# Performance work log

Measured on AMD Instinct MI355X. Metric: run time of the kernel, lower is better.

Reference implementation:

```python
import jax, jax.numpy as jnp
import numpy as np

B, S, N = 16, 512, 321          # batch, input length, n_variates (dec_in)
D, DF, LAYERS = 512, 2048, 2    # d_model, d_ff, e_layers
M, K, P = 3, 3, 96              # wavelet levels, kernel_size, pred_len
ALPHA = 0.3


def _dwconv(x, h, dilation):
    # x: [B, C, L], h: [C, K] depthwise dilated conv (cross-correlation, like torch)
    return jax.lax.conv_general_dilated(
        x, h[:, None, :], window_strides=(1,), padding='VALID',
        rhs_dilation=(dilation,), dimension_numbers=('NCH', 'OIH', 'NCH'),
        feature_group_count=x.shape[1])


def _swt_dec(x, h0, h1):
    # stationary wavelet decomposition; x: [B, N, D] -> [B, N, M+1, D]
    approx, coeffs, dil = x, [], 1
    for _ in range(M):
        pad_total = dil * (K - 1)
        pad_r = (K * dil) // 2
        xp = jnp.pad(approx, ((0, 0), (0, 0), (pad_total - pad_r, pad_r)), mode='wrap')
        coeffs.append(_dwconv(xp, h1, dil))
        approx = _dwconv(xp, h0, dil)
        dil *= 2
    coeffs.append(approx)
    return jnp.stack(coeffs[::-1], axis=-2)


def _swt_rec(c, g0, g1):
    # inverse SWT; c: [B, N, M+1, D] -> [B, N, D]
    approx = c[:, :, 0, :]
    dil = 2 ** (M - 1)
    for i in range(M):
        det = c[:, :, 1 + i, :]
        pad_total = dil * (K - 1)
        pad_l = (dil * K) // 2
        pads = ((0, 0), (0, 0), (pad_l, pad_total - pad_l))
        approx = (_dwconv(jnp.pad(approx, pads, mode='wrap'), g0, dil)
                  + _dwconv(jnp.pad(det, pads, mode='wrap'), g1, dil)) / 2
        dil //= 2
    return approx


def _geom_attention(q, k, v):
    # q,k,v: [B, L=D, H=M+1, E=N]
    scale = 1.0 / jnp.sqrt(jnp.float32(q.shape[-1]))
    dot = jnp.einsum('blhe,bshe->bhls', q, k)
    qn2 = jnp.sum(q * q, -1).transpose(0, 2, 1)  # [B,H,L]
    kn2 = jnp.sum(k * k, -1).transpose(0, 2, 1)  # [B,H,S]
    wedge = jnp.sqrt(jax.nn.relu(qn2[:, :, :, None] * kn2[:, :, None, :] - dot * dot) + 1e-8)
    scores = ((1.0 - ALPHA) * dot + ALPHA * wedge) * scale
    A = jax.nn.softmax(scores, axis=-1)
    return jnp.einsum('bhls,bshd->blhd', A, v)


def _layernorm(x, g, b, eps=1e-5):
    mu = x.mean(-1, keepdims=True)
    var = jnp.mean((x - mu) ** 2, -1, keepdims=True)
    return (x - mu) / jnp.sqrt(var + eps) * g + b


def _forward(x_enc, emb_W, emb_b, h0, h1, g0, g1, Wq, bq, Wk, bk, Wv, bv, Wo, bo,
             W1, b1, W2, b2, ln1_g, ln1_b, ln2_g, ln2_b, lnf_g, lnf_b, proj_W, proj_b):
    # RevIN-style normalize (means detached as in torch code)
    means = jax.lax.stop_gradient(x_enc.mean(1, keepdims=True))
    stdev = jnp.sqrt(x_enc.var(1, keepdims=True) + 1e-5)
    x = (x_enc - means) / stdev
    # inverted embedding: each variate's full series -> d_model token
    h = jnp.einsum('bsn,ds->bnd', x, emb_W) + emb_b  # [B,N,D]
    for l in range(LAYERS):
        coeffs = _swt_dec(h, h0[l], h1[l])  # [B,N,M+1,D]
        q = (jnp.einsum('bnmd,ed->bnme', coeffs, Wq[l]) + bq[l]).transpose(0, 3, 2, 1)
        kk = (jnp.einsum('bnmd,ed->bnme', coeffs, Wk[l]) + bk[l]).transpose(0, 3, 2, 1)
        vv = (jnp.einsum('bnmd,ed->bnme', coeffs, Wv[l]) + bv[l]).transpose(0, 3, 2, 1)
        out = _geom_attention(q, kk, vv).transpose(0, 3, 2, 1)  # [B,N,M+1,D]
        out = _swt_rec(out, g0[l], g1[l])                        # [B,N,D]
        out = jnp.einsum('bnd,ed->bne', out, Wo[l]) + bo[l]
        x1 = _layernorm(h + out, ln1_g[l], ln1_b[l])
        y = jax.nn.gelu(jnp.einsum('bnd,fd->bnf', x1, W1[l]) + b1[l], approximate=False)
        y = jnp.einsum('bnf,df->bnd', y, W2[l]) + b2[l]
        h = _layernorm(x1 + y, ln2_g[l], ln2_b[l])
    h = _layernorm(h, lnf_g, lnf_b)
    dec = (jnp.einsum('bnd,pd->bnp', h, proj_W) + proj_b).transpose(0, 2, 1)  # [B,P,N]
    dec = dec * stdev[:, 0, :][:, None, :] + means[:, 0, :][:, None, :]
    return dec, means, stdev


def setup_inputs():
    key = jax.random.key(0)
    ks = jax.random.split(key, 24)
    def filt(k):
        f = jax.random.normal(k, (LAYERS, N, K), jnp.float32)
        return f / jnp.linalg.norm(f, axis=-1, keepdims=True)
    w = lambda k, shape: jax.random.normal(k, shape, jnp.float32) * 0.02
    z = lambda shape: jnp.zeros(shape, jnp.float32)
    o = lambda shape: jnp.ones(shape, jnp.float32)
    return {
        'x_enc': jax.random.normal(ks[0], (B, S, N), jnp.float32),
        'emb_W': w(ks[1], (D, S)), 'emb_b': z((D,)),
        'h0': filt(ks[2]), 'h1': filt(ks[3]), 'g0': filt(ks[4]), 'g1': filt(ks[5]),
        'Wq': w(ks[6], (LAYERS, D, D)), 'bq': z((LAYERS, D)),
        'Wk': w(ks[7], (LAYERS, D, D)), 'bk': z((LAYERS, D)),
        'Wv': w(ks[8], (LAYERS, D, D)), 'bv': z((LAYERS, D)),
        'Wo': w(ks[9], (LAYERS, D, D)), 'bo': z((LAYERS, D)),
        'W1': w(ks[10], (LAYERS, DF, D)), 'b1': z((LAYERS, DF)),
        'W2': w(ks[11], (LAYERS, D, DF)), 'b2': z((LAYERS, D)),
        'ln1_g': o((LAYERS, D)), 'ln1_b': z((LAYERS, D)),
        'ln2_g': o((LAYERS, D)), 'ln2_b': z((LAYERS, D)),
        'lnf_g': o((D,)), 'lnf_b': z((D,)),
        'proj_W': w(ks[12], (P, D)), 'proj_b': z((P,)),
    }


def reference(x_enc, emb_W, emb_b, h0, h1, g0, g1, Wq, bq, Wk, bk, Wv, bv, Wo, bo,
              W1, b1, W2, b2, ln1_g, ln1_b, ln2_g, ln2_b, lnf_g, lnf_b, proj_W, proj_b):
    return _forward(x_enc, emb_W, emb_b, h0, h1, g0, g1, Wq, bq, Wk, bk, Wv, bv, Wo, bo,
                    W1, b1, W2, b2, ln1_g, ln1_b, ln2_g, ln2_b, lnf_g, lnf_b, proj_W, proj_b)
```

## Files before the change

kernel.cpp:

```cpp
#include <hip/hip_runtime.h>
#include <hip/hip_bf16.h>
#include <math.h>
#include <stdint.h>

#define Bn 16
#define Sn 512
#define Nn 321
#define Dn 512
#define DFn 2048
#define Pn 96
#define KP 352

typedef __bf16 bf16x8 __attribute__((ext_vector_type(8)));
typedef float f32x4 __attribute__((ext_vector_type(4)));
typedef __hip_bfloat16 bf16;

static __device__ __forceinline__ float gelu_exact(float x) {
    return 0.5f * x * (1.0f + erff(x * 0.7071067811865476f));
}

static __device__ __forceinline__ void gld16(const void* g, void* l) {
    __builtin_amdgcn_global_load_lds(
        (const __attribute__((address_space(1))) void*)(uintptr_t)g,
        (__attribute__((address_space(3))) void*)(uintptr_t)l, 16, 0, 0);
}

struct CvtPack {
    const float* src[14];
    bf16* dst[14];
    int cnt[14];
};
__global__ void cvt_all_kernel(CvtPack p) {
    int seg = blockIdx.y;
    int n = p.cnt[seg];
    const float* s = p.src[seg];
    bf16* d = p.dst[seg];
    int i = (blockIdx.x * 256 + threadIdx.x) * 4;
    if (i + 3 < n) {
        float4 v = *reinterpret_cast<const float4*>(s + i);
        d[i] = __float2bfloat16(v.x);
        d[i + 1] = __float2bfloat16(v.y);
        d[i + 2] = __float2bfloat16(v.z);
        d[i + 3] = __float2bfloat16(v.w);
    }
}

__global__ void stats_kernel(const float* __restrict__ x, float* __restrict__ means,
                             float* __restrict__ stdev) {
    int b = blockIdx.y;
    int n = blockIdx.x * 256 + threadIdx.x;
    if (n >= Nn) return;
    const float* p = x + (size_t)b * Sn * Nn + n;
    float s = 0.f, s2 = 0.f;
    for (int ss = 0; ss < Sn; ++ss) { float v = p[(size_t)ss * Nn]; s += v; s2 += v * v; }
    float mu = s * (1.0f / Sn);
    float var = s2 * (1.0f / Sn) - mu * mu;
    means[b * Nn + n] = mu;
    stdev[b * Nn + n] = sqrtf(var + 1e-5f);
}

__global__ void transpose_norm_kernel(const float* __restrict__ x,
                                      const float* __restrict__ means,
                                      const float* __restrict__ stdev,
                                      bf16* __restrict__ xT) {
    __shared__ float tile[32][33];
    int b = blockIdx.z;
    int s0 = blockIdx.x * 32, n0 = blockIdx.y * 32;
    int tx = threadIdx.x, ty = threadIdx.y;
#pragma unroll
    for (int u = 0; u < 4; ++u) {
        int srow = ty + u * 8;
        int n = n0 + tx;
        tile[srow][tx] = (n < Nn) ? x[((size_t)b * Sn + (s0 + srow)) * Nn + n] : 0.f;
    }
    __syncthreads();
#pragma unroll
    for (int u = 0; u < 4; ++u) {
        int n = n0 + ty + u * 8;
        int s = s0 + tx;
        if (n < Nn) {
            float mu = means[b * Nn + n], sd = stdev[b * Nn + n];
            xT[((size_t)b * Nn + n) * Sn + s] = __float2bfloat16((tile[tx][ty + u * 8] - mu) / sd);
        }
    }
}

template <int OUT, int EPI>
__global__ __launch_bounds__(256) void mm_kernel(
    const bf16* __restrict__ A, const bf16* __restrict__ Bm,
    const float* __restrict__ bias, void* __restrict__ C,
    int Mdim, int Ndim, int Kdim, int lda, int ldb, int ldc,
    long sAi, long sAo, long sBi, long sBo, long sCi, long sCo, int innerB) {
    int z = blockIdx.z;
    int zi = z % innerB, zo = z / innerB;
    const bf16* Ab = A + (size_t)zi * sAi + (size_t)zo * sAo;
    const bf16* Bb = Bm + (size_t)zi * sBi + (size_t)zo * sBo;
    __shared__ __align__(16) bf16 As[128 * 32];
    __shared__ __align__(16) bf16 Bs[128 * 32];
    int t = threadIdx.x;
    int wave = t >> 6, lane = t & 63;
    int wr = wave >> 1, wc = wave & 1;
    int q = lane >> 4, l16 = lane & 15;
    int i0 = blockIdx.y * 128, j0 = blockIdx.x * 128;

    int srow0 = t >> 2;
    int scol = (t & 3) * 8;
    f32x4 acc[4][4] = {};

    for (int k0 = 0; k0 < Kdim; k0 += 32) {
#pragma unroll
        for (int u = 0; u < 2; ++u) {
            int row = u * 64 + srow0;
            int gcol = scol ^ (((row >> 1) & 3) << 3);
            int gi = i0 + row; if (gi >= Mdim) gi = Mdim - 1;
            gld16(Ab + (size_t)gi * lda + k0 + gcol, &As[u * 2048 + wave * 512]);
            int gj = j0 + row; if (gj >= Ndim) gj = Ndim - 1;
            gld16(Bb + (size_t)gj * ldb + k0 + gcol, &Bs[u * 2048 + wave * 512]);
        }
        __syncthreads();
        bf16x8 af[4], bfr[4];
#pragma unroll
        for (int mi = 0; mi < 4; ++mi) {
            int r = wr * 64 + mi * 16 + l16;
            int cl = (q * 8) ^ (((r >> 1) & 3) << 3);
            af[mi] = *reinterpret_cast<const bf16x8*>(&As[r * 32 + cl]);
        }
#pragma unroll
        for (int ni = 0; ni < 4; ++ni) {
            int r = wc * 64 + ni * 16 + l16;
            int cl = (q * 8) ^ (((r >> 1) & 3) << 3);
            bfr[ni] = *reinterpret_cast<const bf16x8*>(&Bs[r * 32 + cl]);
        }
#pragma unroll
        for (int mi = 0; mi < 4; ++mi)
#pragma unroll
            for (int ni = 0; ni < 4; ++ni)
                acc[mi][ni] = __builtin_amdgcn_mfma_f32_16x16x32_bf16(af[mi], bfr[ni], acc[mi][ni], 0, 0, 0);
        __syncthreads();
    }
    size_t cbase = (size_t)zi * sCi + (size_t)zo * sCo;
#pragma unroll
    for (int mi = 0; mi < 4; ++mi) {
#pragma unroll
        for (int r = 0; r < 4; ++r) {
            int gi = i0 + wr * 64 + mi * 16 + q * 4 + r;
            if (gi >= Mdim) continue;
#pragma unroll
            for (int ni = 0; ni < 4; ++ni) {
                int gj = j0 + wc * 64 + ni * 16 + l16;
                if (gj >= Ndim) continue;
                float v = acc[mi][ni][r];
                if (bias) v += bias[gj];
                if (EPI == 1) v = gelu_exact(v);
                size_t cidx = cbase + (size_t)gi * ldc + gj;
                if (OUT == 0) ((float*)C)[cidx] = v;
                else ((bf16*)C)[cidx] = __float2bfloat16(v);
            }
        }
    }
}

__global__ __launch_bounds__(128) void swt_dec_kernel(
    const float* __restrict__ h, const float* __restrict__ h0f,
    const float* __restrict__ h1f, bf16* __restrict__ coeffs) {
    __shared__ float a[2][512];
    int b = blockIdx.y, n = blockIdx.x, t = threadIdx.x;
    const float* hrow = h + ((size_t)b * Nn + n) * Dn;
#pragma unroll
    for (int u = 0; u < 4; ++u) a[0][t + u * 128] = hrow[t + u * 128];
    float f0[3], f1[3];
#pragma unroll
    for (int k = 0; k < 3; ++k) { f0[k] = h0f[n * 3 + k]; f1[k] = h1f[n * 3 + k]; }
    __syncthreads();
    bf16* cb = coeffs + ((size_t)b * Nn + n) * 4 * Dn;
    int cur = 0;
    for (int lev = 0; lev < 3; ++lev) {
        int dil = 1 << lev;
        int pl = 2 * dil - (3 * dil) / 2;
#pragma unroll
        for (int u = 0; u < 4; ++u) {
            int d = t + u * 128;
            float dv = 0.f, av = 0.f;
#pragma unroll
            for (int k = 0; k < 3; ++k) {
                int idx = (d + k * dil - pl) & 511;
                float xv = a[cur][idx];
                dv += f1[k] * xv;
                av += f0[k] * xv;
            }
            cb[(size_t)(3 - lev) * Dn + d] = __float2bfloat16(dv);
            a[cur ^ 1][d] = av;
        }
        __syncthreads();
        cur ^= 1;
    }
#pragma unroll
    for (int u = 0; u < 4; ++u) cb[t + u * 128] = __float2bfloat16(a[cur][t + u * 128]);
}

__global__ __launch_bounds__(128) void swt_rec_kernel(
    const bf16* __restrict__ attn, const float* __restrict__ g0f,
    const float* __restrict__ g1f, bf16* __restrict__ rec) {
    __shared__ float a[2][512];
    __shared__ float det[512];
    int b = blockIdx.y, n = blockIdx.x, t = threadIdx.x;
    const bf16* base = attn + ((size_t)(b * 4) * Nn + n) * Dn;
#pragma unroll
    for (int u = 0; u < 4; ++u) a[0][t + u * 128] = __bfloat162float(base[t + u * 128]);
    float w0[3], w1[3];
#pragma unroll
    for (int k = 0; k < 3; ++k) { w0[k] = g0f[n * 3 + k]; w1[k] = g1f[n * 3 + k]; }
    int cur = 0;
    for (int i = 0; i < 3; ++i) {
        int dil = 4 >> i;
        int pl = (3 * dil) / 2;
        const bf16* drow = base + (size_t)(1 + i) * Nn * Dn;
#pragma unroll
        for (int u = 0; u < 4; ++u) det[t + u * 128] = __bfloat162float(drow[t + u * 128]);
        __syncthreads();
#pragma unroll
        for (int u = 0; u < 4; ++u) {
            int d = t + u * 128;
            float s = 0.f;
#pragma unroll
            for (int k = 0; k < 3; ++k) {
                int idx = (d + k * dil - pl) & 511;
                s += w0[k] * a[cur][idx] + w1[k] * det[idx];
            }
            a[cur ^ 1][d] = s * 0.5f;
        }
        __syncthreads();
        cur ^= 1;
    }
    bf16* out = rec + ((size_t)b * Nn + n) * Dn;
#pragma unroll
    for (int u = 0; u < 4; ++u) out[t + u * 128] = __float2bfloat16(a[cur][t + u * 128]);
}

__global__ void tconv_kernel(const bf16* __restrict__ in, bf16* __restrict__ out) {
    __shared__ bf16 tile[32][33];
    int bm = blockIdx.z;
    int b = bm >> 2, m = bm & 3;
    int e0 = blockIdx.x * 32, n0 = blockIdx.y * 32;
    int tx = threadIdx.x, ty = threadIdx.y;
    const bf16* ib = in + (size_t)b * 4 * Nn * 512 + (size_t)m * 512;
    bf16* ob = out + (size_t)bm * 512 * KP;
#pragma unroll
    for (int u = 0; u < 4; ++u) {
        int n = n0 + ty + u * 8;
        bf16 v = __float2bfloat16(0.f);
        if (n < Nn) v = ib[(size_t)n * 2048 + e0 + tx];
        tile[ty + u * 8][tx] = v;
    }
    __syncthreads();
#pragma unroll
    for (int u = 0; u < 4; ++u) {
        int e = e0 + ty + u * 8;
        int n = n0 + tx;
        if (n < KP) ob[(size_t)e * KP + n] = tile[tx][ty + u * 8];
    }
}

__global__ __launch_bounds__(256) void colsq_kernel(const bf16* __restrict__ Q0,
                                                    float* __restrict__ outv) {
    int bm = blockIdx.y;
    int b = bm >> 2, m = bm & 3;
    int e0 = blockIdx.x * 64;
    int tx = threadIdx.x & 63, ty = threadIdx.x >> 6;
    const bf16* base = Q0 + ((size_t)b * Nn * 4 + m) * 512;
    float s = 0.f;
    for (int n = ty; n < Nn; n += 4) {
        float v = __bfloat162float(base[(size_t)n * 2048 + e0 + tx]);
        s += v * v;
    }
    __shared__ float red[4][64];
    red[ty][tx] = s;
    __syncthreads();
    if (ty == 0)
        outv[(size_t)bm * 512 + e0 + tx] = red[0][tx] + red[1][tx] + red[2][tx] + red[3][tx];
}

__global__ __launch_bounds__(256) void wedge_softmax_kernel(
    bf16* __restrict__ Smat, const float* __restrict__ qn2, const float* __restrict__ kn2) {
    int bm = blockIdx.y, l = blockIdx.x, t = threadIdx.x;
    bf16* row = Smat + ((size_t)bm * 512 + l) * 512;
    const float* kn = kn2 + (size_t)bm * 512;
    float q2 = qn2[(size_t)bm * 512 + l];
    const float scale = rsqrtf(321.0f);
    float v[2];
    float mx = -1e30f;
#pragma unroll
    for (int u = 0; u < 2; ++u) {
        int s = t + u * 256;
        float d = __bfloat162float(row[s]);
        float w = sqrtf(fmaxf(q2 * kn[s] - d * d, 0.f) + 1e-8f);
        float sc = (0.7f * d + 0.3f * w) * scale;
        v[u] = sc;
        mx = fmaxf(mx, sc);
    }
    __shared__ float red[256];
    red[t] = mx;
    __syncthreads();
    for (int o = 128; o > 0; o >>= 1) {
        if (t < o) red[t] = fmaxf(red[t], red[t + o]);
        __syncthreads();
    }
    mx = red[0];
    __syncthreads();
    float sum = 0.f;
#pragma unroll
    for (int u = 0; u < 2; ++u) {
        v[u] = expf(v[u] - mx);
        sum += v[u];
    }
    red[t] = sum;
    __syncthreads();
    for (int o = 128; o > 0; o >>= 1) {
        if (t < o) red[t] += red[t + o];
        __syncthreads();
    }
    float inv = 1.0f / red[0];
#pragma unroll
    for (int u = 0; u < 2; ++u) row[t + u * 256] = __float2bfloat16(v[u] * inv);
}

__global__ __launch_bounds__(128) void ln_kernel(
    const float* __restrict__ A, const float* __restrict__ R,
    const float* __restrict__ g, const float* __restrict__ bb,
    float* __restrict__ outf, bf16* __restrict__ outb) {
    size_t r = blockIdx.x;
    int t = threadIdx.x;
    const float* ra = A + r * Dn;
    float x[4];
    float s = 0.f, s2 = 0.f;
#pragma unroll
    for (int u = 0; u < 4; ++u) {
        int d = t + u * 128;
        float v = ra[d];
        if (R) v += R[r * Dn + d];
        x[u] = v;
        s += v;
        s2 += v * v;
    }
    __shared__ float rs[128], rs2[128];
    rs[t] = s;
    rs2[t] = s2;
    __syncthreads();
    for (int o = 64; o > 0; o >>= 1) {
        if (t < o) { rs[t] += rs[t + o]; rs2[t] += rs2[t + o]; }
        __syncthreads();
    }
    float mean = rs[0] * (1.0f / Dn);
    float var = rs2[0] * (1.0f / Dn) - mean * mean;
    float inv = rsqrtf(var + 1e-5f);
#pragma unroll
    for (int u = 0; u < 4; ++u) {
        int d = t + u * 128;
        float v = (x[u] - mean) * inv * g[d] + bb[d];
        if (outf) outf[r * Dn + d] = v;
        if (outb) outb[r * Dn + d] = __float2bfloat16(v);
    }
}

__global__ void out_scale_kernel(const float* __restrict__ ptmp,
                                 const float* __restrict__ means,
                                 const float* __restrict__ stdev, float* __restrict__ dec) {
    int idx = blockIdx.x * 256 + threadIdx.x;
    if (idx >= Bn * Pn * Nn) return;
    int n = idx % Nn;
    int bp = idx / Nn;
    int p = bp % Pn;
    int b = bp / Pn;
    float v = ptmp[((size_t)b * Nn + n) * Pn + p];
    dec[idx] = v * stdev[b * Nn + n] + means[b * Nn + n];
}

extern "C" void kernel_launch(void* const* d_in, const int* in_sizes, int n_in,
                              void* d_out, int out_size, void* d_ws, size_t ws_size,
                              hipStream_t stream) {
    const float* x_enc = (const float*)d_in[0];
    const float* emb_W = (const float*)d_in[1];
    const float* emb_b = (const float*)d_in[2];
    const float* h0 = (const float*)d_in[3];
    const float* h1 = (const float*)d_in[4];
    const float* g0 = (const float*)d_in[5];
    const float* g1 = (const float*)d_in[6];
    const float* Wq = (const float*)d_in[7];
    const float* bq = (const float*)d_in[8];
    const float* Wk = (const float*)d_in[9];
    const float* bk = (const float*)d_in[10];
    const float* Wv = (const float*)d_in[11];
    const float* bv = (const float*)d_in[12];
    const float* Wo = (const float*)d_in[13];
    const float* bo = (const float*)d_in[14];
    const float* W1 = (const float*)d_in[15];
    const float* b1 = (const float*)d_in[16];
    const float* W2 = (const float*)d_in[17];
    const float* b2 = (const float*)d_in[18];
    const float* ln1_g = (const float*)d_in[19];
    const float* ln1_b = (const float*)d_in[20];
    const float* ln2_g = (const float*)d_in[21];
    const float* ln2_b = (const float*)d_in[22];
    const float* lnf_g = (const float*)d_in[23];
    const float* lnf_b = (const float*)d_in[24];
    const float* proj_W = (const float*)d_in[25];
    const float* proj_b = (const float*)d_in[26];

    float* dec = (float*)d_out;
    float* means = dec + (size_t)Bn * Pn * Nn;
    float* stdev = means + (size_t)Bn * Nn;

    char* p = (char*)d_ws;
    auto alloc = [&](size_t bytes) { char* r = p; p += (bytes + 255) & ~(size_t)255; return r; };
    const size_t RD = (size_t)Bn * Nn * Dn;
    const size_t RQ4 = RD * 4;

    bf16* embWb = (bf16*)alloc(262144 * 2);
    bf16* Wqb = (bf16*)alloc(2 * 262144 * 2);
    bf16* Wkb = (bf16*)alloc(2 * 262144 * 2);
    bf16* Wvb = (bf16*)alloc(2 * 262144 * 2);
    bf16* Wob = (bf16*)alloc(2 * 262144 * 2);
    bf16* W1b = (bf16*)alloc(2 * 1048576 * 2);
    bf16* W2b = (bf16*)alloc(2 * 1048576 * 2);
    bf16* projWb = (bf16*)alloc(49152 * 2);

    float* hbuf = (float*)alloc(RD * 4);
    char* regC = alloc(RQ4 * 2);
    char* regQ = alloc(RQ4 * 2);
    char* regK = alloc(RQ4 * 2);
    char* regV = alloc(RQ4 * 2);
    char* regT = alloc((size_t)2 * 64 * 512 * KP * 2);
    float* qn2 = (float*)alloc(64 * 512 * 4);
    float* kn2 = (float*)alloc(64 * 512 * 4);

    bf16* coeffs_b = (bf16*)regC;
    bf16* attn_b = (bf16*)regC;
    bf16* Q0b = (bf16*)regQ;
    bf16* Smat = (bf16*)regQ;
    bf16* recb = (bf16*)regQ;
    bf16* x1b = (bf16*)(regQ + RD * 2);
    float* ptmp = (float*)regQ;
    bf16* K0b = (bf16*)regK;
    bf16* V0b = (bf16*)regV;
    bf16* yb = (bf16*)regV;
    bf16* Qt = (bf16*)regT;
    bf16* Kt = Qt + (size_t)64 * 512 * KP;
    bf16* xT_b = (bf16*)regT;
    float* x1 = (float*)regT;
    float* tmp = (float*)(regT + RD * 4);
    bf16* hfb = (bf16*)(regT + RD * 8);

    const int R = Bn * Nn;
    const int RQr = R * 4;
    const long sbm = (long)4 * Nn * 512;
    const long sS = (long)512 * 512;
    const long sTq = (long)512 * KP;
    const long sTb = 4 * sTq;

    CvtPack cp;
    int ci = 0;
    auto addcvt = [&](const float* s, bf16* d, int n) { cp.src[ci] = s; cp.dst[ci] = d; cp.cnt[ci] = n; ++ci; };
    addcvt(emb_W, embWb, 262144);
    for (int l = 0; l < 2; ++l) {
        addcvt(Wq + (size_t)l * 262144, Wqb + (size_t)l * 262144, 262144);
        addcvt(Wk + (size_t)l * 262144, Wkb + (size_t)l * 262144, 262144);
        addcvt(Wv + (size_t)l * 262144, Wvb + (size_t)l * 262144, 262144);
        addcvt(Wo + (size_t)l * 262144, Wob + (size_t)l * 262144, 262144);
        addcvt(W1 + (size_t)l * 1048576, W1b + (size_t)l * 1048576, 1048576);
        addcvt(W2 + (size_t)l * 1048576, W2b + (size_t)l * 1048576, 1048576);
    }
    addcvt(proj_W, projWb, 49152);
    cvt_all_kernel<<<dim3(1048576 / 4 / 256, 14), 256, 0, stream>>>(cp);

    stats_kernel<<<dim3((Nn + 255) / 256, Bn), 256, 0, stream>>>(x_enc, means, stdev);
    transpose_norm_kernel<<<dim3(Sn / 32, (Nn + 31) / 32, Bn), dim3(32, 8), 0, stream>>>(
        x_enc, means, stdev, xT_b);

    mm_kernel<0, 0><<<dim3(4, (R + 127) / 128, 1), 256, 0, stream>>>(
        xT_b, embWb, emb_b, hbuf, R, Dn, Sn, Sn, Sn, Dn, 0, 0, 0, 0, 0, 0, 1);

    for (int l = 0; l < 2; ++l) {
        const float* h0l = h0 + (size_t)l * Nn * 3;
        const float* h1l = h1 + (size_t)l * Nn * 3;
        const float* g0l = g0 + (size_t)l * Nn * 3;
        const float* g1l = g1 + (size_t)l * Nn * 3;

        swt_dec_kernel<<<dim3(Nn, Bn), 128, 0, stream>>>(hbuf, h0l, h1l, coeffs_b);

        mm_kernel<1, 0><<<dim3(4, (RQr + 127) / 128, 1), 256, 0, stream>>>(
            coeffs_b, Wqb + (size_t)l * 262144, bq + (size_t)l * Dn, Q0b,
            RQr, Dn, Dn, Dn, Dn, Dn, 0, 0, 0, 0, 0, 0, 1);
        mm_kernel<1, 0><<<dim3(4, (RQr + 127) / 128, 1), 256, 0, stream>>>(
            coeffs_b, Wkb + (size_t)l * 262144, bk + (size_t)l * Dn, K0b,
            RQr, Dn, Dn, Dn, Dn, Dn, 0, 0, 0, 0, 0, 0, 1);
        mm_kernel<1, 0><<<dim3(4, (RQr + 127) / 128, 1), 256, 0, stream>>>(
            coeffs_b, Wvb + (size_t)l * 262144, bv + (size_t)l * Dn, V0b,
            RQr, Dn, Dn, Dn, Dn, Dn, 0, 0, 0, 0, 0, 0, 1);

        colsq_kernel<<<dim3(8, 64), 256, 0, stream>>>(Q0b, qn2);
        colsq_kernel<<<dim3(8, 64), 256, 0, stream>>>(K0b, kn2);
        tconv_kernel<<<dim3(16, 11, 64), dim3(32, 8), 0, stream>>>(Q0b, Qt);
        tconv_kernel<<<dim3(16, 11, 64), dim3(32, 8), 0, stream>>>(K0b, Kt);

        mm_kernel<1, 0><<<dim3(4, 4, 64), 256, 0, stream>>>(
            Qt, Kt, nullptr, Smat, 512, 512, KP, KP, KP, 512,
            sTq, sTb, sTq, sTb, sS, 4 * sS, 4);

        wedge_softmax_kernel<<<dim3(512, 64), 256, 0, stream>>>(Smat, qn2, kn2);

        mm_kernel<1, 0><<<dim3(4, (Nn + 127) / 128, 64), 256, 0, stream>>>(
            V0b, Smat, nullptr, attn_b, Nn, 512, 512, 2048, 512, 512,
            512, sbm, sS, 4 * sS, (long)Nn * 512, (long)4 * Nn * 512, 4);

        swt_rec_kernel<<<dim3(Nn, Bn), 128, 0, stream>>>(attn_b, g0l, g1l, recb);

        mm_kernel<0, 0><<<dim3(4, (R + 127) / 128, 1), 256, 0, stream>>>(
            recb, Wob + (size_t)l * 262144, bo + (size_t)l * Dn, tmp,
            R, Dn, Dn, Dn, Dn, Dn, 0, 0, 0, 0, 0, 0, 1);
        ln_kernel<<<R, 128, 0, stream>>>(hbuf, tmp, ln1_g + (size_t)l * Dn,
                                         ln1_b + (size_t)l * Dn, x1, x1b);

        mm_kernel<1, 1><<<dim3(16, (R + 127) / 128, 1), 256, 0, stream>>>(
            x1b, W1b + (size_t)l * 1048576, b1 + (size_t)l * DFn, yb,
            R, DFn, Dn, Dn, Dn, DFn, 0, 0, 0, 0, 0, 0, 1);
        mm_kernel<0, 0><<<dim3(4, (R + 127) / 128, 1), 256, 0, stream>>>(
            yb, W2b + (size_t)l * 1048576, b2 + (size_t)l * Dn, tmp,
            R, Dn, DFn, DFn, DFn, Dn, 0, 0, 0, 0, 0, 0, 1);
        ln_kernel<<<R, 128, 0, stream>>>(x1, tmp, ln2_g + (size_t)l * Dn,
                                         ln2_b + (size_t)l * Dn, hbuf, nullptr);
    }

    ln_kernel<<<R, 128, 0, stream>>>(hbuf, nullptr, lnf_g, lnf_b, nullptr, hfb);
    mm_kernel<0, 0><<<dim3(1, (R + 127) / 128, 1), 256, 0, stream>>>(
        hfb, projWb, proj_b, ptmp, R, Pn, Dn, Dn, Dn, Pn, 0, 0, 0, 0, 0, 0, 1);
    out_scale_kernel<<<(Bn * Pn * Nn + 255) / 256, 256, 0, stream>>>(ptmp, means, stdev, dec);
}
```

Before: 1.092 ms.

## Fuse Q/K projections into one GEMM and split-K narrow GEMMs

Wq and Wk are packed into one weight, with a packed bias, so one N=1024 GEMM produces an interleaved QK buffer. The column-norm and transpose kernels are merged to handle Q and K in a single launch each. The Wo, W2 and final projection GEMMs are split along K (2, 2 and 4 ways) into separate partial buffers. LayerNorm and the output-scaling kernel sum those partials. This targets launch overhead and the low block count of the narrow GEMMs, at the cost of extra partial-sum traffic and workspace, and a risk of the bias being added once per split.

Measured after the change: 1.003 ms. 1.09x faster.

```diff
diff --git a/kernel.cpp b/kernel.cpp
--- a/kernel.cpp
+++ b/kernel.cpp
@@ -45,6 +45,14 @@
     }
 }
 
+__global__ void bias_pack_kernel(const float* __restrict__ bq, const float* __restrict__ bk,
+                                 float* __restrict__ bqk) {
+    int idx = blockIdx.x * 256 + threadIdx.x;
+    if (idx >= 2048) return;
+    int l = idx >> 10, j = idx & 1023;
+    bqk[idx] = (j < 512) ? bq[l * 512 + j] : bk[l * 512 + j - 512];
+}
+
 __global__ void stats_kernel(const float* __restrict__ x, float* __restrict__ means,
                              float* __restrict__ stdev) {
     int b = blockIdx.y;
@@ -237,19 +245,20 @@
     for (int u = 0; u < 4; ++u) out[t + u * 128] = __float2bfloat16(a[cur][t + u * 128]);
 }
 
-__global__ void tconv_kernel(const bf16* __restrict__ in, bf16* __restrict__ out) {
+__global__ void tconv2_kernel(const bf16* __restrict__ QK, bf16* __restrict__ QtKt) {
     __shared__ bf16 tile[32][33];
-    int bm = blockIdx.z;
+    int zz = blockIdx.z;
+    int qk = zz >> 6, bm = zz & 63;
     int b = bm >> 2, m = bm & 3;
     int e0 = blockIdx.x * 32, n0 = blockIdx.y * 32;
     int tx = threadIdx.x, ty = threadIdx.y;
-    const bf16* ib = in + (size_t)b * 4 * Nn * 512 + (size_t)m * 512;
-    bf16* ob = out + (size_t)bm * 512 * KP;
+    const bf16* ib = QK + (size_t)b * Nn * 4096 + (size_t)m * 1024 + (size_t)qk * 512;
+    bf16* ob = QtKt + (size_t)qk * 64 * 512 * KP + (size_t)bm * 512 * KP;
 #pragma unroll
     for (int u = 0; u < 4; ++u) {
         int n = n0 + ty + u * 8;
         bf16 v = __float2bfloat16(0.f);
-        if (n < Nn) v = ib[(size_t)n * 2048 + e0 + tx];
+        if (n < Nn) v = ib[(size_t)n * 4096 + e0 + tx];
         tile[ty + u * 8][tx] = v;
     }
     __syncthreads();
@@ -261,23 +270,25 @@
     }
 }
 
-__global__ __launch_bounds__(256) void colsq_kernel(const bf16* __restrict__ Q0,
-                                                    float* __restrict__ outv) {
-    int bm = blockIdx.y;
+__global__ __launch_bounds__(256) void colsq2_kernel(const bf16* __restrict__ QK,
+                                                     float* __restrict__ outv) {
+    int y = blockIdx.y;
+    int qk = y >> 6, bm = y & 63;
     int b = bm >> 2, m = bm & 3;
     int e0 = blockIdx.x * 64;
     int tx = threadIdx.x & 63, ty = threadIdx.x >> 6;
-    const bf16* base = Q0 + ((size_t)b * Nn * 4 + m) * 512;
+    const bf16* base = QK + ((size_t)b * Nn * 4 + m) * 1024 + (size_t)qk * 512;
     float s = 0.f;
     for (int n = ty; n < Nn; n += 4) {
-        float v = __bfloat162float(base[(size_t)n * 2048 + e0 + tx]);
+        float v = __bfloat162float(base[(size_t)n * 4096 + e0 + tx]);
         s += v * v;
     }
     __shared__ float red[4][64];
     red[ty][tx] = s;
     __syncthreads();
     if (ty == 0)
-        outv[(size_t)bm * 512 + e0 + tx] = red[0][tx] + red[1][tx] + red[2][tx] + red[3][tx];
+        outv[(size_t)qk * 32768 + (size_t)bm * 512 + e0 + tx] =
+            red[0][tx] + red[1][tx] + red[2][tx] + red[3][tx];
 }
 
 __global__ __launch_bounds__(256) void wedge_softmax_kernel(
@@ -325,7 +336,7 @@
 }
 
 __global__ __launch_bounds__(128) void ln_kernel(
-    const float* __restrict__ A, const float* __restrict__ R,
+    const float* __restrict__ A, const float* __restrict__ R, const float* __restrict__ R2,
     const float* __restrict__ g, const float* __restrict__ bb,
     float* __restrict__ outf, bf16* __restrict__ outb) {
     size_t r = blockIdx.x;
@@ -338,6 +349,7 @@
         int d = t + u * 128;
         float v = ra[d];
         if (R) v += R[r * Dn + d];
+        if (R2) v += R2[r * Dn + d];
         x[u] = v;
         s += v;
         s2 += v * v;
@@ -371,7 +383,9 @@
     int bp = idx / Nn;
     int p = bp % Pn;
     int b = bp / Pn;
-    float v = ptmp[((size_t)b * Nn + n) * Pn + p];
+    const size_t PS = (size_t)Bn * Nn * Pn;
+    size_t base = ((size_t)b * Nn + n) * Pn + p;
+    float v = ptmp[base] + ptmp[base + PS] + ptmp[base + 2 * PS] + ptmp[base + 3 * PS];
     dec[idx] = v * stdev[b * Nn + n] + means[b * Nn + n];
 }
 
@@ -416,13 +430,13 @@
     const size_t RQ4 = RD * 4;
 
     bf16* embWb = (bf16*)alloc(262144 * 2);
-    bf16* Wqb = (bf16*)alloc(2 * 262144 * 2);
-    bf16* Wkb = (bf16*)alloc(2 * 262144 * 2);
+    bf16* Wqkb = (bf16*)alloc(2 * 524288 * 2);
     bf16* Wvb = (bf16*)alloc(2 * 262144 * 2);
     bf16* Wob = (bf16*)alloc(2 * 262144 * 2);
     bf16* W1b = (bf16*)alloc(2 * 1048576 * 2);
     bf16* W2b = (bf16*)alloc(2 * 1048576 * 2);
     bf16* projWb = (bf16*)alloc(49152 * 2);
+    float* bqk = (float*)alloc(2048 * 4);
 
     float* hbuf = (float*)alloc(RD * 4);
     char* regC = alloc(RQ4 * 2);
@@ -430,25 +444,25 @@
     char* regK = alloc(RQ4 * 2);
     char* regV = alloc(RQ4 * 2);
     char* regT = alloc((size_t)2 * 64 * 512 * KP * 2);
-    float* qn2 = (float*)alloc(64 * 512 * 4);
-    float* kn2 = (float*)alloc(64 * 512 * 4);
+    float* qn2 = (float*)alloc((size_t)2 * 64 * 512 * 4);
+    float* kn2 = qn2 + 32768;
 
     bf16* coeffs_b = (bf16*)regC;
     bf16* attn_b = (bf16*)regC;
-    bf16* Q0b = (bf16*)regQ;
+    bf16* QK0b = (bf16*)regQ;
     bf16* Smat = (bf16*)regQ;
     bf16* recb = (bf16*)regQ;
     bf16* x1b = (bf16*)(regQ + RD * 2);
     float* ptmp = (float*)regQ;
-    bf16* K0b = (bf16*)regK;
     bf16* V0b = (bf16*)regV;
     bf16* yb = (bf16*)regV;
-    bf16* Qt = (bf16*)regT;
-    bf16* Kt = Qt + (size_t)64 * 512 * KP;
+    bf16* QtKt = (bf16*)regT;
+    bf16* Qt = QtKt;
+    bf16* Kt = QtKt + (size_t)64 * 512 * KP;
     bf16* xT_b = (bf16*)regT;
     float* x1 = (float*)regT;
     float* tmp = (float*)(regT + RD * 4);
-    bf16* hfb = (bf16*)(regT + RD * 8);
+    bf16* hfb = (bf16*)(regT + RD * 12);
 
     const int R = Bn * Nn;
     const int RQr = R * 4;
@@ -462,8 +476,8 @@
     auto addcvt = [&](const float* s, bf16* d, int n) { cp.src[ci] = s; cp.dst[ci] = d; cp.cnt[ci] = n; ++ci; };
     addcvt(emb_W, embWb, 262144);
     for (int l = 0; l < 2; ++l) {
-        addcvt(Wq + (size_t)l * 262144, Wqb + (size_t)l * 262144, 262144);
-        addcvt(Wk + (size_t)l * 262144, Wkb + (size_t)l * 262144, 262144);
+        addcvt(Wq + (size_t)l * 262144, Wqkb + (size_t)l * 524288, 262144);
+        addcvt(Wk + (size_t)l * 262144, Wqkb + (size_t)l * 524288 + 262144, 262144);
         addcvt(Wv + (size_t)l * 262144, Wvb + (size_t)l * 262144, 262144);
         addcvt(Wo + (size_t)l * 262144, Wob + (size_t)l * 262144, 262144);
         addcvt(W1 + (size_t)l * 1048576, W1b + (size_t)l * 1048576, 1048576);
@@ -471,6 +485,7 @@
     }
     addcvt(proj_W, projWb, 49152);
     cvt_all_kernel<<<dim3(1048576 / 4 / 256, 14), 256, 0, stream>>>(cp);
+    bias_pack_kernel<<<8, 256, 0, stream>>>(bq, bk, bqk);
 
     stats_kernel<<<dim3((Nn + 255) / 256, Bn), 256, 0, stream>>>(x_enc, means, stdev);
     transpose_norm_kernel<<<dim3(Sn / 32, (Nn + 31) / 32, Bn), dim3(32, 8), 0, stream>>>(
@@ -487,20 +502,15 @@
 
         swt_dec_kernel<<<dim3(Nn, Bn), 128, 0, stream>>>(hbuf, h0l, h1l, coeffs_b);
 
-        mm_kernel<1, 0><<<dim3(4, (RQr + 127) / 128, 1), 256, 0, stream>>>(
-            coeffs_b, Wqb + (size_t)l * 262144, bq + (size_t)l * Dn, Q0b,
-            RQr, Dn, Dn, Dn, Dn, Dn, 0, 0, 0, 0, 0, 0, 1);
-        mm_kernel<1, 0><<<dim3(4, (RQr + 127) / 128, 1), 256, 0, stream>>>(
-            coeffs_b, Wkb + (size_t)l * 262144, bk + (size_t)l * Dn, K0b,
-            RQr, Dn, Dn, Dn, Dn, Dn, 0, 0, 0, 0, 0, 0, 1);
+        mm_kernel<1, 0><<<dim3(8, (RQr + 127) / 128, 1), 256, 0, stream>>>(
+            coeffs_b, Wqkb + (size_t)l * 524288, bqk + (size_t)l * 1024, QK0b,
+            RQr, 1024, Dn, Dn, Dn, 1024, 0, 0, 0, 0, 0, 0, 1);
         mm_kernel<1, 0><<<dim3(4, (RQr + 127) / 128, 1), 256, 0, stream>>>(
             coeffs_b, Wvb + (size_t)l * 262144, bv + (size_t)l * Dn, V0b,
             RQr, Dn, Dn, Dn, Dn, Dn, 0, 0, 0, 0, 0, 0, 1);
 
-        colsq_kernel<<<dim3(8, 64), 256, 0, stream>>>(Q0b, qn2);
-        colsq_kernel<<<dim3(8, 64), 256, 0, stream>>>(K0b, kn2);
-        tconv_kernel<<<dim3(16, 11, 64), dim3(32, 8), 0, stream>>>(Q0b, Qt);
-        tconv_kernel<<<dim3(16, 11, 64), dim3(32, 8), 0, stream>>>(K0b, Kt);
+        colsq2_kernel<<<dim3(8, 128), 256, 0, stream>>>(QK0b, qn2);
+        tconv2_kernel<<<dim3(16, 11, 128), dim3(32, 8), 0, stream>>>(QK0b, QtKt);
 
         mm_kernel<1, 0><<<dim3(4, 4, 64), 256, 0, stream>>>(
             Qt, Kt, nullptr, Smat, 512, 512, KP, KP, KP, 512,
@@ -514,24 +524,25 @@
 
         swt_rec_kernel<<<dim3(Nn, Bn), 128, 0, stream>>>(attn_b, g0l, g1l, recb);
 
-        mm_kernel<0, 0><<<dim3(4, (R + 127) / 128, 1), 256, 0, stream>>>(
+        mm_kernel<0, 0><<<dim3(4, (R + 127) / 128, 2), 256, 0, stream>>>(
             recb, Wob + (size_t)l * 262144, bo + (size_t)l * Dn, tmp,
-            R, Dn, Dn, Dn, Dn, Dn, 0, 0, 0, 0, 0, 0, 1);
-        ln_kernel<<<R, 128, 0, stream>>>(hbuf, tmp, ln1_g + (size_t)l * Dn,
+            R, Dn, 256, Dn, Dn, Dn, 256, 0, 256, 0, (long)RD, 0, 2);
+        ln_kernel<<<R, 128, 0, stream>>>(hbuf, tmp, tmp + RD, ln1_g + (size_t)l * Dn,
                                          ln1_b + (size_t)l * Dn, x1, x1b);
 
         mm_kernel<1, 1><<<dim3(16, (R + 127) / 128, 1), 256, 0, stream>>>(
             x1b, W1b + (size_t)l * 1048576, b1 + (size_t)l * DFn, yb,
             R, DFn, Dn, Dn, Dn, DFn, 0, 0, 0, 0, 0, 0, 1);
-        mm_kernel<0, 0><<<dim3(4, (R + 127) / 128, 1), 256, 0, stream>>>(
+        mm_kernel<0, 0><<<dim3(4, (R + 127) / 128, 2), 256, 0, stream>>>(
             yb, W2b + (size_t)l * 1048576, b2 + (size_t)l * Dn, tmp,
-            R, Dn, DFn, DFn, DFn, Dn, 0, 0, 0, 0, 0, 0, 1);
-        ln_kernel<<<R, 128, 0, stream>>>(x1, tmp, ln2_g + (size_t)l * Dn,
+            R, Dn, 1024, DFn, DFn, Dn, 1024, 0, 1024, 0, (long)RD, 0, 2);
+        ln_kernel<<<R, 128, 0, stream>>>(x1, tmp, tmp + RD, ln2_g + (size_t)l * Dn,
                                          ln2_b + (size_t)l * Dn, hbuf, nullptr);
     }
 
-    ln_kernel<<<R, 128, 0, stream>>>(hbuf, nullptr, lnf_g, lnf_b, nullptr, hfb);
-    mm_kernel<0, 0><<<dim3(1, (R + 127) / 128, 1), 256, 0, stream>>>(
-        hfb, projWb, proj_b, ptmp, R, Pn, Dn, Dn, Dn, Pn, 0, 0, 0, 0, 0, 0, 1);
+    ln_kernel<<<R, 128, 0, stream>>>(hbuf, nullptr, nullptr, lnf_g, lnf_b, nullptr, hfb);
+    mm_kernel<0, 0><<<dim3(1, (R + 127) / 128, 4), 256, 0, stream>>>(
+        hfb, projWb, proj_b, ptmp, R, Pn, 128, Dn, Dn, Pn,
+        128, 0, 128, 0, (long)R * Pn, 0, 4);
     out_scale_kernel<<<(Bn * Pn * Nn + 255) / 256, 256, 0, stream>>>(ptmp, means, stdev, dec);
 }
```
